# Performance work log

Measured on AMD Instinct MI355X. Metric: run time of the kernel, lower is better.

Reference implementation:

```python
import jax, jax.numpy as jnp
import numpy as np
from jax import lax

# sRGB linear -> LMS matrix (Oklab M1)
M1 = jnp.array([[0.4122214708, 0.5363325363, 0.0514459929],
                [0.2119034982, 0.6806995451, 0.1073969566],
                [0.0883024619, 0.2817188376, 0.6299787005]], dtype=jnp.float32)
# LMS^(1/3) -> Oklab matrix (Oklab M2)
M2 = jnp.array([[0.2104542553, 0.7936177850, -0.0040720468],
                [1.9779984951, -2.4285922050, 0.4505937099],
                [0.0259040371, 0.7827717662, -0.8086757660]], dtype=jnp.float32)
_SX = jnp.array([[-1., 0., 1.], [-2., 0., 2.], [-1., 0., 1.]], dtype=jnp.float32)
_SY = jnp.array([[-1., -2., -1.], [0., 0., 0.], [1., 2., 1.]], dtype=jnp.float32)
SOBEL = jnp.stack([_SX, _SY])[:, None]  # (2,1,3,3) cross-correlation kernels

CLOSING_KERNEL = 11
CLOSING_PAD = CLOSING_KERNEL // 2
EDGE_THRESHOLD = 0.5
POST_DILATION = 2
EPS = 0.01


def _srgb_to_linear(srgb):
    srgb = jnp.clip(srgb, 0.0, 1.0)
    return jnp.where(srgb <= 0.04045, srgb / 12.92, ((srgb + 0.055) / 1.055) ** 2.4)


def _rgb_to_oklab(rgb):  # [B,3,H,W] -> [B,3,H,W]
    linear = _srgb_to_linear(rgb)
    lms = jnp.einsum('oc,bchw->bohw', M1, linear)
    lms = jnp.clip(lms, 1e-10, None) ** (1.0 / 3.0)
    return jnp.einsum('oc,bchw->bohw', M2, lms)


def _max_pool(x, k, p):  # torch max_pool2d pads with -inf implicitly
    return lax.reduce_window(x, -jnp.inf, lax.max, (1, 1, k, k), (1, 1, 1, 1),
                             [(0, 0), (0, 0), (p, p), (p, p)])


def _min_pool(x, k, p):  # -max_pool(-x): padding becomes +inf
    return lax.reduce_window(x, jnp.inf, lax.min, (1, 1, k, k), (1, 1, 1, 1),
                             [(0, 0), (0, 0), (p, p), (p, p)])


def _omni_edge(img):  # [B,C,H,W] -> [B,1,H,W]
    B, C, H, W = img.shape
    flat = img.reshape(B * C, 1, H, W)
    g = lax.conv_general_dilated(flat, SOBEL, (1, 1), [(1, 1), (1, 1)])  # [B*C,2,H,W]
    grad = (jnp.abs(g[:, 0]) + jnp.abs(g[:, 1])).reshape(B, C, H, W)
    return jnp.max(grad, axis=1, keepdims=True)


def _crevice_mask(target):
    edge_soft = jnp.clip(_omni_edge(target) / EDGE_THRESHOLD, 0.0, 1.0)
    dilated = _max_pool(edge_soft, CLOSING_KERNEL, CLOSING_PAD)
    closed = _min_pool(dilated, CLOSING_KERNEL, CLOSING_PAD)
    mask = jax.nn.relu(closed - edge_soft)
    if POST_DILATION > 0:
        dk = 2 * POST_DILATION + 1
        mask = _max_pool(mask, dk, POST_DILATION)
    return mask


def setup_inputs() -> dict:
    key = jax.random.key(0)
    k1, k2 = jax.random.split(key)
    shape = (8, 3, 1024, 1024)
    pred = jax.random.uniform(k1, shape, dtype=jnp.float32)
    target = jax.random.uniform(k2, shape, dtype=jnp.float32)
    return {"pred": pred, "target": target}


def reference(pred, target):
    crevice_mask = _crevice_mask(target)
    mask_sum = jnp.maximum(crevice_mask.sum(), 1.0)
    pred_lab = _rgb_to_oklab(pred)
    target_lab = _rgb_to_oklab(target)
    p_a, p_b = pred_lab[:, 1:2], pred_lab[:, 2:3]
    t_a, t_b = target_lab[:, 1:2], target_lab[:, 2:3]
    C_pred = jnp.sqrt(p_a ** 2 + p_b ** 2 + 1e-12)
    C_gt = jnp.sqrt(t_a ** 2 + t_b ** 2 + 1e-12)
    chroma_loss = (jnp.abs(C_pred - C_gt) * crevice_mask).sum() / mask_sum
    dot_ab = p_a * t_a + p_b * t_b
    cos_hue_diff = jnp.clip(dot_ab / (C_pred * C_gt + 1e-12), -1.0, 1.0)
    hue_loss = (jnp.clip(C_gt, EPS, None) * (1.0 - cos_hue_diff) * crevice_mask).sum() / mask_sum
    return chroma_loss + 2.0 * hue_loss
```

## Files before the change

kernel.cpp:

```cpp
#include <hip/hip_runtime.h>
#include <math.h>

#define K1_NR 16
#define SROWS 64
#define PCH   16
#define QCAP  1024


__device__ __forceinline__ float srgb_to_linear(float x) {
    x = fminf(fmaxf(x, 0.0f), 1.0f);
    return (x <= 0.04045f) ? x * (1.0f / 12.92f)
                           : powf((x + 0.055f) * (1.0f / 1.055f), 2.4f);
}

__device__ __forceinline__ void oklab_ab(float r, float g, float b,
                                         float& A, float& Bc) {
    r = srgb_to_linear(r);
    g = srgb_to_linear(g);
    b = srgb_to_linear(b);
    float l = 0.4122214708f * r + 0.5363325363f * g + 0.0514459929f * b;
    float m = 0.2119034982f * r + 0.6806995451f * g + 0.1073969566f * b;
    float s = 0.0883024619f * r + 0.2817188376f * g + 0.6299787005f * b;
    l = cbrtf(fmaxf(l, 1e-10f));
    m = cbrtf(fmaxf(m, 1e-10f));
    s = cbrtf(fmaxf(s, 1e-10f));
    A  = 1.9779984951f * l - 2.428592205f * m + 0.4505937099f * s;
    Bc = 0.0259040371f * l + 0.7827717662f * m - 0.808675766f  * s;
}

__device__ __forceinline__ void color_terms(const float* __restrict__ pred,
                                            const float* __restrict__ target,
                                            size_t off, size_t HWp, float m,
                                            float& sc, float& sh) {
    float pa, pb, ta, tb;
    oklab_ab(pred[off], pred[off + HWp], pred[off + 2 * HWp], pa, pb);
    oklab_ab(target[off], target[off + HWp], target[off + 2 * HWp], ta, tb);
    float Cp = sqrtf(pa * pa + pb * pb + 1e-12f);
    float Cg = sqrtf(ta * ta + tb * tb + 1e-12f);
    sc += fabsf(Cp - Cg) * m;
    float cosd = (pa * ta + pb * tb) / (Cp * Cg + 1e-12f);
    cosd = fminf(fmaxf(cosd, -1.0f), 1.0f);
    sh += fmaxf(Cg, 0.01f) * (1.0f - cosd) * m;
}


__device__ __forceinline__ void k1_load_row(const float* __restrict__ tb,
                                            size_t HW, int c, int r,
                                            int H, int W, int col0,
                                            bool lok, bool rok, int lc, int rc,
                                            float4& m4, float& ml, float& mr) {
    if (r >= 0 && r < H) {
        const float* rp = tb + (size_t)c * HW + (size_t)r * W;
        m4 = *(const float4*)(rp + col0);
        ml = lok ? rp[lc] : 0.f;
        mr = rok ? rp[rc] : 0.f;
    } else {
        m4 = make_float4(0.f, 0.f, 0.f, 0.f);
        ml = 0.f; mr = 0.f;
    }
}

__device__ __forceinline__ float4 k1_sobel_g(const float4& pr, const float4& cu,
                                             const float4& nx,
                                             float lpr, float lcu, float lnx,
                                             float rpr, float rcu, float rnx) {
    float4 u, v;
    u.x = fmaf(2.f, cu.x, pr.x) + nx.x;
    u.y = fmaf(2.f, cu.y, pr.y) + nx.y;
    u.z = fmaf(2.f, cu.z, pr.z) + nx.z;
    u.w = fmaf(2.f, cu.w, pr.w) + nx.w;
    v.x = nx.x - pr.x; v.y = nx.y - pr.y;
    v.z = nx.z - pr.z; v.w = nx.w - pr.w;
    float ul = fmaf(2.f, lcu, lpr) + lnx;
    float vl = lnx - lpr;
    float ur = fmaf(2.f, rcu, rpr) + rnx;
    float vr = rnx - rpr;
    float4 g;
    g.x = fabsf(u.y - ul)  + fabsf(fmaf(2.f, v.x, vl) + v.y);
    g.y = fabsf(u.z - u.x) + fabsf(fmaf(2.f, v.y, v.x) + v.z);
    g.z = fabsf(u.w - u.y) + fabsf(fmaf(2.f, v.z, v.y) + v.w);
    g.w = fabsf(ur - u.z)  + fabsf(fmaf(2.f, v.w, v.z) + vr);
    return g;
}

__global__ __launch_bounds__(256) void k1_edge(const float* __restrict__ target,
                                               float* __restrict__ edge,
                                               int H, int W) {
    int strips = H / K1_NR;
    int b   = blockIdx.x / strips;
    int ysi = blockIdx.x % strips;
    int t   = threadIdx.x;
    int col0 = t << 2;
    int y0 = ysi * K1_NR;
    int yend = y0 + K1_NR - 1;
    size_t HW = (size_t)H * W;
    const float* tb = target + (size_t)b * 3 * HW;
    float* ep = edge + (size_t)b * HW + col0;

    bool lok = (col0 > 0);
    bool rok = (col0 + 4 < W);
    int lc = lok ? col0 - 1 : 0;
    int rc = rok ? col0 + 4 : W - 1;

    float4 pr[3], cu[3];
    float lpr[3], lcu[3], rpr[3], rcu[3];
#pragma unroll
    for (int c = 0; c < 3; ++c) {
        k1_load_row(tb, HW, c, y0 - c - 1, H, W, col0, lok, rok, lc, rc,
                    pr[c], lpr[c], rpr[c]);
        k1_load_row(tb, HW, c, y0 - c, H, W, col0, lok, rok, lc, rc,
                    cu[c], lcu[c], rcu[c]);
    }

    float4 acc1 = make_float4(0.f, 0.f, 0.f, 0.f);
    float4 acc2 = make_float4(0.f, 0.f, 0.f, 0.f);

    for (int s = y0; s < y0 + K1_NR + 2; ++s) {
        float4 g0 = make_float4(0.f, 0.f, 0.f, 0.f);
#pragma unroll
        for (int c = 0; c < 3; ++c) {
            if (s - c <= yend) {
                float4 nx; float lnx, rnx;
                k1_load_row(tb, HW, c, s - c + 1, H, W, col0, lok, rok, lc, rc,
                            nx, lnx, rnx);
                float4 g = k1_sobel_g(pr[c], cu[c], nx,
                                      lpr[c], lcu[c], lnx,
                                      rpr[c], rcu[c], rnx);
                if (c == 0) {
                    g0 = g;
                } else if (c == 1) {
                    acc1.x = fmaxf(acc1.x, g.x); acc1.y = fmaxf(acc1.y, g.y);
                    acc1.z = fmaxf(acc1.z, g.z); acc1.w = fmaxf(acc1.w, g.w);
                } else {
                    acc2.x = fmaxf(acc2.x, g.x); acc2.y = fmaxf(acc2.y, g.y);
                    acc2.z = fmaxf(acc2.z, g.z); acc2.w = fmaxf(acc2.w, g.w);
                }
                pr[c] = cu[c]; cu[c] = nx;
                lpr[c] = lcu[c]; lcu[c] = lnx;
                rpr[c] = rcu[c]; rcu[c] = rnx;
            }
        }
        if (s >= y0 + 2) {
            float4 e;
            e.x = fminf(2.f * acc2.x, 1.f);
            e.y = fminf(2.f * acc2.y, 1.f);
            e.z = fminf(2.f * acc2.z, 1.f);
            e.w = fminf(2.f * acc2.w, 1.f);
            *(float4*)(ep + (size_t)(s - 2) * W) = e;
        }
        acc2 = acc1;
        acc1 = g0;
    }
}


template <int R, bool ISMAX, bool SUB_EDGE>
__global__ __launch_bounds__(256) void pool_kernel(const float* __restrict__ in,
                                                   const float* __restrict__ edge,
                                                   float* __restrict__ out,
                                                   int H, int W) {
    const int OUTW = 256 - 2 * R;
    __shared__ float s_v[PCH][256];
    int cb = (W + OUTW - 1) / OUTW;
    int rs = H / SROWS;
    int blk = blockIdx.x;
    int b   = blk / (cb * rs);
    int t   = blk % (cb * rs);
    int bxi = t / rs, ysi = t % rs;
    int tid = threadIdx.x;
    int col = bxi * OUTW - R + tid;
    int cc  = min(max(col, 0), W - 1);
    size_t base = (size_t)b * H * W;
    const float* colp = in + base + cc;
    int ys = ysi * SROWS;
    bool writer = (tid >= R) && (tid < OUTW + R) && (col < W);

    for (int ph = 0; ph < SROWS / PCH; ++ph) {
        int y0 = ys + ph * PCH;
        float w[PCH + 2 * R];
#pragma unroll
        for (int k = 0; k < PCH + 2 * R; ++k) {
            int r = min(max(y0 - R + k, 0), H - 1);
            w[k] = colp[(size_t)r * W];
        }
        float v[PCH];
#pragma unroll
        for (int k = 0; k < PCH; ++k) {
            float m = w[k];
#pragma unroll
            for (int d = 1; d <= 2 * R; ++d)
                m = ISMAX ? fmaxf(m, w[k + d]) : fminf(m, w[k + d]);
            v[k] = m;
        }
        __syncthreads();
#pragma unroll
        for (int k = 0; k < PCH; ++k) s_v[k][tid] = v[k];
        __syncthreads();
        if (writer) {
#pragma unroll
            for (int k = 0; k < PCH; ++k) {
                float m = s_v[k][tid - R];
#pragma unroll
                for (int d = 1; d <= 2 * R; ++d)
                    m = ISMAX ? fmaxf(m, s_v[k][tid - R + d])
                              : fminf(m, s_v[k][tid - R + d]);
                size_t gi = base + (size_t)(y0 + k) * W + col;
                out[gi] = SUB_EDGE ? fmaxf(m - edge[gi], 0.f) : m;
            }
        }
    }
}


__global__ __launch_bounds__(256) void k4_loss(const float* __restrict__ pred,
                                               const float* __restrict__ target,
                                               const float* __restrict__ mask0,
                                               float* __restrict__ partials,
                                               int H, int W, int nb) {
    const int R = 2, OUTW = 256 - 2 * R;
    __shared__ float s_v[PCH][256];
    __shared__ int   q_pos[QCAP];
    __shared__ float q_m[QCAP];
    __shared__ int   cnt;
    __shared__ float s_red[3][4];

    int cb = (W + OUTW - 1) / OUTW;
    int rs = H / SROWS;
    int blk = blockIdx.x;
    int b   = blk / (cb * rs);
    int t   = blk % (cb * rs);
    int bxi = t / rs, ysi = t % rs;
    int tid = threadIdx.x;
    int col = bxi * OUTW - R + tid;
    int cc  = min(max(col, 0), W - 1);
    size_t HWp  = (size_t)H * W;
    size_t base = (size_t)b * HWp;
    size_t cbase = (size_t)b * 3 * HWp;
    const float* colp = mask0 + base + cc;
    int ys = ysi * SROWS;
    bool writer = (tid >= R) && (tid < OUTW + R) && (col < W);

    float sm = 0.f, sc = 0.f, sh = 0.f;

    for (int ph = 0; ph < SROWS / PCH; ++ph) {
        int y0 = ys + ph * PCH;
        float w[PCH + 2 * R];
#pragma unroll
        for (int k = 0; k < PCH + 2 * R; ++k) {
            int r = min(max(y0 - R + k, 0), H - 1);
            w[k] = colp[(size_t)r * W];
        }
        float v[PCH];
#pragma unroll
        for (int k = 0; k < PCH; ++k) {
            float m = w[k];
#pragma unroll
            for (int d = 1; d <= 2 * R; ++d) m = fmaxf(m, w[k + d]);
            v[k] = m;
        }
        __syncthreads();
#pragma unroll
        for (int k = 0; k < PCH; ++k) s_v[k][tid] = v[k];
        if (tid == 0) cnt = 0;
        __syncthreads();
        if (writer) {
#pragma unroll
            for (int k = 0; k < PCH; ++k) {
                float m = s_v[k][tid - R];
#pragma unroll
                for (int d = 1; d <= 2 * R; ++d)
                    m = fmaxf(m, s_v[k][tid - R + d]);
                sm += m;
                if (m > 0.f) {
                    int pos = atomicAdd(&cnt, 1);
                    if (pos < QCAP) {
                        q_pos[pos] = ((y0 + k) << 16) | col;
                        q_m[pos] = m;
                    } else {
                        color_terms(pred, target,
                                    cbase + (size_t)(y0 + k) * W + col,
                                    HWp, m, sc, sh);
                    }
                }
            }
        }
        __syncthreads();
        int n = min(cnt, QCAP);
        for (int i = tid; i < n; i += 256) {
            int pk = q_pos[i];
            color_terms(pred, target,
                        cbase + (size_t)(pk >> 16) * W + (pk & 0xffff),
                        HWp, q_m[i], sc, sh);
        }
    }

#pragma unroll
    for (int off = 32; off > 0; off >>= 1) {
        sm += __shfl_down(sm, off);
        sc += __shfl_down(sc, off);
        sh += __shfl_down(sh, off);
    }
    int lane = tid & 63, wav = tid >> 6;
    __syncthreads();
    if (lane == 0) { s_red[0][wav] = sm; s_red[1][wav] = sc; s_red[2][wav] = sh; }
    __syncthreads();
    if (tid == 0) {
        float tm = 0, tc = 0, th = 0;
        for (int i = 0; i < 4; ++i) {
            tm += s_red[0][i]; tc += s_red[1][i]; th += s_red[2][i];
        }
        partials[blk]          = tm;
        partials[nb + blk]     = tc;
        partials[2 * nb + blk] = th;
    }
}

__global__ void finalize_kernel(const float* __restrict__ partials, int nb,
                                float* __restrict__ out) {
    double sm = 0.0, sc = 0.0, sh = 0.0;
    for (int i = threadIdx.x; i < nb; i += blockDim.x) {
        sm += (double)partials[i];
        sc += (double)partials[nb + i];
        sh += (double)partials[2 * nb + i];
    }
    __shared__ double red[3][256];
    red[0][threadIdx.x] = sm;
    red[1][threadIdx.x] = sc;
    red[2][threadIdx.x] = sh;
    __syncthreads();
    for (int s = blockDim.x / 2; s > 0; s >>= 1) {
        if ((int)threadIdx.x < s) {
            red[0][threadIdx.x] += red[0][threadIdx.x + s];
            red[1][threadIdx.x] += red[1][threadIdx.x + s];
            red[2][threadIdx.x] += red[2][threadIdx.x + s];
        }
        __syncthreads();
    }
    if (threadIdx.x == 0) {
        double ms = fmax(red[0][0], 1.0);
        out[0] = (float)(red[1][0] / ms + 2.0 * red[2][0] / ms);
    }
}


extern "C" void kernel_launch(void* const* d_in, const int* in_sizes, int n_in,
                              void* d_out, int out_size, void* d_ws, size_t ws_size,
                              hipStream_t stream) {
    const float* pred   = (const float*)d_in[0];
    const float* target = (const float*)d_in[1];
    float* out = (float*)d_out;

    const int H = 1024, W = 1024;
    int Bn = in_sizes[0] / (3 * H * W);
    size_t plane = (size_t)Bn * H * W * sizeof(float);

    char* ws = (char*)d_ws;
    float* planeA = (float*)ws;
    float* planeB = (float*)(ws + plane);
    float* partials = (float*)(ws + 2 * plane);

    int g1 = Bn * (H / K1_NR);
    int rs = H / SROWS;
    int cbP = (W + 245) / 246;
    int cb4 = (W + 251) / 252;
    int gP = Bn * cbP * rs;
    int g4 = Bn * cb4 * rs;

    k1_edge<<<g1, 256, 0, stream>>>(target, planeA, H, W);
    pool_kernel<5, true, false><<<gP, 256, 0, stream>>>(planeA, nullptr, planeB, H, W);
    pool_kernel<5, false, true><<<gP, 256, 0, stream>>>(planeB, planeA, planeA, H, W);
    k4_loss<<<g4, 256, 0, stream>>>(pred, target, planeA, partials, H, W, g4);
    finalize_kernel<<<1, 256, 0, stream>>>(partials, g4, out);
}
```

Measured before the change: 101.0 us.

## Split Sobel edge kernel across channel wavefronts with shared-memory max reduction

The edge kernel now gives each of three wavefronts one color channel for a 256-column by 8-row tile. Each wavefront loads its rows into registers up front, computes Sobel magnitudes, and writes them to shared memory; after a barrier, all threads take the channel max and store the clamped edge map. This swaps the old per-thread skewed streaming loop over all channels for many more small blocks with independent loads, aiming to raise memory-level parallelism. The cost is a 2-row halo re-read per 8-row strip and extra shared-memory traffic.

```diff
diff --git a/kernel.cpp b/kernel.cpp
--- a/kernel.cpp
+++ b/kernel.cpp
@@ -1,7 +1,7 @@
 #include <hip/hip_runtime.h>
 #include <math.h>
 
-#define K1_NR 16
+#define K1_NR 8
 #define SROWS 64
 #define PCH   16
 #define QCAP  1024
@@ -43,22 +43,6 @@
     sh += fmaxf(Cg, 0.01f) * (1.0f - cosd) * m;
 }
 
-
-__device__ __forceinline__ void k1_load_row(const float* __restrict__ tb,
-                                            size_t HW, int c, int r,
-                                            int H, int W, int col0,
-                                            bool lok, bool rok, int lc, int rc,
-                                            float4& m4, float& ml, float& mr) {
-    if (r >= 0 && r < H) {
-        const float* rp = tb + (size_t)c * HW + (size_t)r * W;
-        m4 = *(const float4*)(rp + col0);
-        ml = lok ? rp[lc] : 0.f;
-        mr = rok ? rp[rc] : 0.f;
-    } else {
-        m4 = make_float4(0.f, 0.f, 0.f, 0.f);
-        ml = 0.f; mr = 0.f;
-    }
-}
 
 __device__ __forceinline__ float4 k1_sobel_g(const float4& pr, const float4& cu,
                                              const float4& nx,
@@ -83,73 +67,61 @@
     return g;
 }
 
-__global__ __launch_bounds__(256) void k1_edge(const float* __restrict__ target,
+__global__ __launch_bounds__(192) void k1_edge(const float* __restrict__ target,
                                                float* __restrict__ edge,
                                                int H, int W) {
+    __shared__ float4 s_g[3][K1_NR][64];
+
     int strips = H / K1_NR;
-    int b   = blockIdx.x / strips;
-    int ysi = blockIdx.x % strips;
-    int t   = threadIdx.x;
-    int col0 = t << 2;
-    int y0 = ysi * K1_NR;
-    int yend = y0 + K1_NR - 1;
+    int cgs = W >> 8;
+    int blk = blockIdx.x;
+    int b   = blk / (strips * cgs);
+    int rem = blk % (strips * cgs);
+    int strip = rem / cgs, cg = rem % cgs;
+    int f0 = strip * K1_NR;
+    int lane = threadIdx.x & 63;
+    int wv   = threadIdx.x >> 6;
+    int col0 = (cg << 8) + (lane << 2);
     size_t HW = (size_t)H * W;
-    const float* tb = target + (size_t)b * 3 * HW;
-    float* ep = edge + (size_t)b * HW + col0;
+    const float* p = target + (size_t)b * 3 * HW + (size_t)wv * HW;
 
     bool lok = (col0 > 0);
     bool rok = (col0 + 4 < W);
     int lc = lok ? col0 - 1 : 0;
-    int rc = rok ? col0 + 4 : W - 1;
-
-    float4 pr[3], cu[3];
-    float lpr[3], lcu[3], rpr[3], rcu[3];
-#pragma unroll
-    for (int c = 0; c < 3; ++c) {
-        k1_load_row(tb, HW, c, y0 - c - 1, H, W, col0, lok, rok, lc, rc,
-                    pr[c], lpr[c], rpr[c]);
-        k1_load_row(tb, HW, c, y0 - c, H, W, col0, lok, rok, lc, rc,
-                    cu[c], lcu[c], rcu[c]);
-    }
-
-    float4 acc1 = make_float4(0.f, 0.f, 0.f, 0.f);
-    float4 acc2 = make_float4(0.f, 0.f, 0.f, 0.f);
-
-    for (int s = y0; s < y0 + K1_NR + 2; ++s) {
-        float4 g0 = make_float4(0.f, 0.f, 0.f, 0.f);
-#pragma unroll
-        for (int c = 0; c < 3; ++c) {
-            if (s - c <= yend) {
-                float4 nx; float lnx, rnx;
-                k1_load_row(tb, HW, c, s - c + 1, H, W, col0, lok, rok, lc, rc,
-                            nx, lnx, rnx);
-                float4 g = k1_sobel_g(pr[c], cu[c], nx,
-                                      lpr[c], lcu[c], lnx,
-                                      rpr[c], rcu[c], rnx);
-                if (c == 0) {
-                    g0 = g;
-                } else if (c == 1) {
-                    acc1.x = fmaxf(acc1.x, g.x); acc1.y = fmaxf(acc1.y, g.y);
-                    acc1.z = fmaxf(acc1.z, g.z); acc1.w = fmaxf(acc1.w, g.w);
-                } else {
-                    acc2.x = fmaxf(acc2.x, g.x); acc2.y = fmaxf(acc2.y, g.y);
-                    acc2.z = fmaxf(acc2.z, g.z); acc2.w = fmaxf(acc2.w, g.w);
-                }
-                pr[c] = cu[c]; cu[c] = nx;
-                lpr[c] = lcu[c]; lcu[c] = lnx;
-                rpr[c] = rcu[c]; rcu[c] = rnx;
-            }
-        }
-        if (s >= y0 + 2) {
-            float4 e;
-            e.x = fminf(2.f * acc2.x, 1.f);
-            e.y = fminf(2.f * acc2.y, 1.f);
-            e.z = fminf(2.f * acc2.z, 1.f);
-            e.w = fminf(2.f * acc2.w, 1.f);
-            *(float4*)(ep + (size_t)(s - 2) * W) = e;
-        }
-        acc2 = acc1;
-        acc1 = g0;
+    int rc = rok ? col0 + 4 : 0;
+
+    float4 w[K1_NR + 2];
+    float wl[K1_NR + 2], wr[K1_NR + 2];
+#pragma unroll
+    for (int i = 0; i < K1_NR + 2; ++i) {
+        int r = f0 - 1 + i;
+        bool oky = (r >= 0) && (r < H);
+        const float* rp = p + (size_t)r * W;
+        w[i]  = oky ? *(const float4*)(rp + col0)
+                    : make_float4(0.f, 0.f, 0.f, 0.f);
+        wl[i] = (oky && lok) ? rp[lc] : 0.f;
+        wr[i] = (oky && rok) ? rp[rc] : 0.f;
+    }
+#pragma unroll
+    for (int k = 0; k < K1_NR; ++k) {
+        s_g[wv][k][lane] = k1_sobel_g(w[k], w[k + 1], w[k + 2],
+                                      wl[k], wl[k + 1], wl[k + 2],
+                                      wr[k], wr[k + 1], wr[k + 2]);
+    }
+    __syncthreads();
+
+    float* ep = edge + (size_t)b * HW + (size_t)(cg << 8);
+    for (int i = threadIdx.x; i < K1_NR * 64; i += 192) {
+        int row = i >> 6, l = i & 63;
+        float4 g0 = s_g[0][row][l];
+        float4 g1 = s_g[1][row][l];
+        float4 g2 = s_g[2][row][l];
+        float4 e;
+        e.x = fminf(2.f * fmaxf(g0.x, fmaxf(g1.x, g2.x)), 1.f);
+        e.y = fminf(2.f * fmaxf(g0.y, fmaxf(g1.y, g2.y)), 1.f);
+        e.z = fminf(2.f * fmaxf(g0.z, fmaxf(g1.z, g2.z)), 1.f);
+        e.w = fminf(2.f * fmaxf(g0.w, fmaxf(g1.w, g2.w)), 1.f);
+        *(float4*)(ep + (size_t)(f0 + row) * W + (l << 2)) = e;
     }
 }
 
@@ -359,14 +331,14 @@
     float* planeB = (float*)(ws + plane);
     float* partials = (float*)(ws + 2 * plane);
 
-    int g1 = Bn * (H / K1_NR);
+    int g1 = Bn * (H / K1_NR) * (W >> 8);
     int rs = H / SROWS;
     int cbP = (W + 245) / 246;
     int cb4 = (W + 251) / 252;
     int gP = Bn * cbP * rs;
     int g4 = Bn * cb4 * rs;
 
-    k1_edge<<<g1, 256, 0, stream>>>(target, planeA, H, W);
+    k1_edge<<<g1, 192, 0, stream>>>(target, planeA, H, W);
     pool_kernel<5, true, false><<<gP, 256, 0, stream>>>(planeA, nullptr, planeB, H, W);
     pool_kernel<5, false, true><<<gP, 256, 0, stream>>>(planeB, planeA, planeA, H, W);
     k4_loss<<<g4, 256, 0, stream>>>(pred, target, planeA, partials, H, W, g4);
```

Result: slower. 103.1 us (+2.1%).
